# Optimization experiments

Hardware: AMD Instinct MI355X
Metric: run time of the kernel (lower is better)

The kernel has to match this reference:

```python
import jax, jax.numpy as jnp
import numpy as np

B, N, F_IN, F_HID, F_OUT = 64, 1024, 64, 128, 64

def setup_inputs() -> dict:
    key = jax.random.key(0)
    ks = jax.random.split(key, 6)
    x = jax.random.normal(ks[0], (B, N, F_IN), dtype=jnp.float32)
    adj = jax.random.uniform(ks[1], (B, N, N), dtype=jnp.float32)
    mask = jax.random.randint(ks[2], (B, N), 0, 2).astype(bool)
    W1 = jax.random.normal(ks[3], (F_IN, F_HID), dtype=jnp.float32) * (1.0 / np.sqrt(F_IN))
    b1 = jnp.zeros((F_HID,), dtype=jnp.float32)
    W2 = jax.random.normal(ks[4], (F_HID, F_OUT), dtype=jnp.float32) * (1.0 / np.sqrt(F_HID))
    b2 = jnp.zeros((F_OUT,), dtype=jnp.float32)
    eps = jnp.zeros((1,), dtype=jnp.float32)
    return {"x": x, "adj": adj, "mask": mask, "W1": W1, "b1": b1, "W2": W2, "b2": b2, "eps": eps}

def reference(x, adj, mask, W1, b1, W2, b2, eps):
    # neighbor aggregation: out[b,i,f] = sum_j adj[b,i,j] * x[b,j,f]
    agg = jnp.einsum('bij,bjf->bif', adj, x)
    # add_loop=True: (1 + eps) * x + aggregated neighbors
    h = (1.0 + eps[0]) * x + agg
    # 2-layer GIN MLP applied per node (only valid nodes contribute in the
    # torch version via gather/scatter; invalid positions are zeroed)
    h = jax.nn.relu(h @ W1 + b1) @ W2 + b2
    return jnp.where(mask[..., None], h, jnp.zeros((), dtype=h.dtype))
```

## Files before the change

### kernel.cpp

```cpp
#include <hip/hip_runtime.h>


#define N_    1024
#define FIN   64
#define FHID  128
#define FOUT  64
#define HS_LD 68
#define H1_LD 132
#define FROW  9

typedef __attribute__((ext_vector_type(16))) float f32x16;
typedef __attribute__((ext_vector_type(8)))  short s16x8;

__device__ inline short f2bf(float f) {
    union { float f; unsigned int u; } v; v.f = f;
    unsigned int r = v.u + 0x7fffu + ((v.u >> 16) & 1u);
    return (short)(r >> 16);
}

__global__ __launch_bounds__(256) void gin_fused(
    const float* __restrict__ x, const float* __restrict__ adj,
    const int* __restrict__ mask, const float* __restrict__ W1,
    const float* __restrict__ b1, const float* __restrict__ W2,
    const float* __restrict__ b2, const float* __restrict__ epsp,
    float* __restrict__ out)
{
    __shared__ s16x8 region1[2112];
    __shared__ float hs[64 * HS_LD];

    s16x8 (*asf)[FROW] = reinterpret_cast<s16x8 (*)[FROW]>(region1);
    s16x8 (*xtf)[FROW] = reinterpret_cast<s16x8 (*)[FROW]>(region1 + 576);
    float* h1s = reinterpret_cast<float*>(region1);

    const int t    = threadIdx.x;
    const int lane = t & 63;
    const int w    = t >> 6;
    const int b    = blockIdx.x >> 4;
    const int i0   = (blockIdx.x & 15) * 64;

    const float* xb   = x   + (size_t)b * N_ * FIN;
    const float* adjb = adj + (size_t)b * N_ * N_ + (size_t)i0 * N_;

    const int l31  = lane & 31;
    const int half = lane >> 5;
    const int mrow = (w & 1) * 32;
    const int ncol = (w >> 1) * 32;

    const int sr = t >> 2;
    const int sc = (t & 3) * 16;
    const int sg = (t & 3) * 2;

    f32x16 acc;
    #pragma unroll
    for (int r = 0; r < 16; ++r) acc[r] = 0.f;

    for (int jc = 0; jc < N_ / 64; ++jc) {
        const int j0 = jc * 64;

        {
            const float* ar = adjb + (size_t)sr * N_ + j0 + sc;
            const float4 p0 = *reinterpret_cast<const float4*>(ar);
            const float4 p1 = *reinterpret_cast<const float4*>(ar + 4);
            const float4 p2 = *reinterpret_cast<const float4*>(ar + 8);
            const float4 p3 = *reinterpret_cast<const float4*>(ar + 12);
            s16x8 f0, f1;
            f0[0] = f2bf(p0.x); f0[1] = f2bf(p0.y); f0[2] = f2bf(p0.z); f0[3] = f2bf(p0.w);
            f0[4] = f2bf(p1.x); f0[5] = f2bf(p1.y); f0[6] = f2bf(p1.z); f0[7] = f2bf(p1.w);
            f1[0] = f2bf(p2.x); f1[1] = f2bf(p2.y); f1[2] = f2bf(p2.z); f1[3] = f2bf(p2.w);
            f1[4] = f2bf(p3.x); f1[5] = f2bf(p3.y); f1[6] = f2bf(p3.z); f1[7] = f2bf(p3.w);
            asf[sr][sg]     = f0;
            asf[sr][sg + 1] = f1;
        }
        {
            s16x8 q0, q1;
            #pragma unroll
            for (int jj = 0; jj < 8; ++jj)
                q0[jj] = f2bf(xb[(size_t)(j0 + w * 16 + jj) * FIN + lane]);
            #pragma unroll
            for (int jj = 0; jj < 8; ++jj)
                q1[jj] = f2bf(xb[(size_t)(j0 + w * 16 + 8 + jj) * FIN + lane]);
            xtf[lane][2 * w]     = q0;
            xtf[lane][2 * w + 1] = q1;
        }
        __syncthreads();

        #pragma unroll
        for (int s = 0; s < 4; ++s) {
            const s16x8 a  = asf[mrow + l31][2 * s + half];
            const s16x8 bf = xtf[ncol + l31][2 * s + half];
            acc = __builtin_amdgcn_mfma_f32_32x32x16_bf16(a, bf, acc, 0, 0, 0);
        }
        __syncthreads();
    }

    {
        const float se = 1.0f + epsp[0];
        const int col = ncol + l31;
        #pragma unroll
        for (int reg = 0; reg < 16; ++reg) {
            const int row = mrow + (reg & 3) + 8 * (reg >> 2) + 4 * half;
            const float xv = xb[(size_t)(i0 + row) * FIN + col];
            hs[row * HS_LD + col] = acc[reg] + se * xv;
        }
    }
    __syncthreads();

    {
        const int k4 = (t & 31) * 4;
        const int rb = (t >> 5) * 8;
        float4 hacc[8];
        const float4 b1v = *reinterpret_cast<const float4*>(b1 + k4);
        #pragma unroll
        for (int r = 0; r < 8; ++r) hacc[r] = b1v;

        #pragma unroll 4
        for (int j = 0; j < FIN; ++j) {
            const float4 w1v = *reinterpret_cast<const float4*>(W1 + j * FHID + k4);
            #pragma unroll
            for (int r = 0; r < 8; ++r) {
                const float hv = hs[(rb + r) * HS_LD + j];
                hacc[r].x += hv * w1v.x; hacc[r].y += hv * w1v.y;
                hacc[r].z += hv * w1v.z; hacc[r].w += hv * w1v.w;
            }
        }
        #pragma unroll
        for (int r = 0; r < 8; ++r) {
            float4 v;
            v.x = fmaxf(hacc[r].x, 0.f); v.y = fmaxf(hacc[r].y, 0.f);
            v.z = fmaxf(hacc[r].z, 0.f); v.w = fmaxf(hacc[r].w, 0.f);
            *reinterpret_cast<float4*>(&h1s[(rb + r) * H1_LD + k4]) = v;
        }
    }
    __syncthreads();

    {
        const int fi = (t & 15) * 4;
        const int ri = (t >> 4) * 4;
        float4 oacc[4];
        const float4 b2v = *reinterpret_cast<const float4*>(b2 + fi);
        #pragma unroll
        for (int ii = 0; ii < 4; ++ii) oacc[ii] = b2v;

        #pragma unroll 4
        for (int j = 0; j < FHID; ++j) {
            const float4 w2v = *reinterpret_cast<const float4*>(W2 + j * FOUT + fi);
            #pragma unroll
            for (int ii = 0; ii < 4; ++ii) {
                const float hv = h1s[(ri + ii) * H1_LD + j];
                oacc[ii].x += hv * w2v.x; oacc[ii].y += hv * w2v.y;
                oacc[ii].z += hv * w2v.z; oacc[ii].w += hv * w2v.w;
            }
        }
        #pragma unroll
        for (int ii = 0; ii < 4; ++ii) {
            const int gi = i0 + ri + ii;
            const int m  = mask[b * N_ + gi];
            float4 o = oacc[ii];
            if (!m) o = make_float4(0.f, 0.f, 0.f, 0.f);
            *reinterpret_cast<float4*>(out + ((size_t)b * N_ + gi) * FOUT + fi) = o;
        }
    }
}

extern "C" void kernel_launch(void* const* d_in, const int* in_sizes, int n_in,
                              void* d_out, int out_size, void* d_ws, size_t ws_size,
                              hipStream_t stream) {
    const float* x    = (const float*)d_in[0];
    const float* adj  = (const float*)d_in[1];
    const int*   mask = (const int*)  d_in[2];
    const float* W1   = (const float*)d_in[3];
    const float* b1   = (const float*)d_in[4];
    const float* W2   = (const float*)d_in[5];
    const float* b2   = (const float*)d_in[6];
    const float* eps  = (const float*)d_in[7];
    float* out = (float*)d_out;

    dim3 grid(64 * 16);
    dim3 block(256);
    gin_fused<<<grid, block, 0, stream>>>(x, adj, mask, W1, b1, W2, b2, eps, out);
}
```

Measured before the change: 428.4 us.

## Pre-pack x and weights to bf16 fragments, stream adj directly, MFMA for MLP

Adds pre-pass kernels that convert x into transposed bf16 MFMA fragments and pack W1/W2 into bf16 fragments in workspace. The main kernel now loads adj straight from global memory into MFMA A-fragments, with no LDS staging and no per-chunk barriers. Both MLP layers move from scalar FP32 FMAs to bf16 MFMA, and launch bounds request higher occupancy. This removes redundant per-block x conversion and barrier stalls, but adds extra launches, workspace traffic and bf16 rounding in the MLP.

New measurement: 440.7 us. +2.9%, slower.

```diff
diff --git a/kernel.cpp b/kernel.cpp
--- a/kernel.cpp
+++ b/kernel.cpp
@@ -5,9 +5,7 @@
 #define FIN   64
 #define FHID  128
 #define FOUT  64
-#define HS_LD 68
-#define H1_LD 132
-#define FROW  9
+#define HROW  136
 
 typedef __attribute__((ext_vector_type(16))) float f32x16;
 typedef __attribute__((ext_vector_type(8)))  short s16x8;
@@ -18,19 +16,66 @@
     return (short)(r >> 16);
 }
 
-__global__ __launch_bounds__(256) void gin_fused(
+__global__ __launch_bounds__(256) void xt_pack(const float* __restrict__ x,
+                                               s16x8* __restrict__ xt)
+{
+    const int g  = blockIdx.x * 256 + threadIdx.x;
+    const int n  = g & 31;
+    const int ng = (g >> 5) & 1;
+    const int ks = (g >> 6) & 63;
+    const int b  = g >> 12;
+    const int f  = ng * 32 + n;
+
+    s16x8 u0, u1;
+    #pragma unroll
+    for (int k = 0; k < 8; ++k)
+        u0[k] = f2bf(x[(size_t)(b * N_ + ks * 16 + k) * FIN + f]);
+    #pragma unroll
+    for (int k = 0; k < 8; ++k)
+        u1[k] = f2bf(x[(size_t)(b * N_ + ks * 16 + 8 + k) * FIN + f]);
+    xt[2 * g]     = u0;
+    xt[2 * g + 1] = u1;
+}
+
+__global__ __launch_bounds__(256) void w_pack(const float* __restrict__ W1,
+                                              const float* __restrict__ W2,
+                                              s16x8* __restrict__ w1f,
+                                              s16x8* __restrict__ w2f)
+{
+    const int g = blockIdx.x * 256 + threadIdx.x;
+    const int u    = g & 63;
+    const int n    = u >> 1;
+    const int half = u & 1;
+    if (g < 1024) {
+        const int ng = (g >> 6) & 3;
+        const int ks = g >> 8;
+        s16x8 fr;
+        #pragma unroll
+        for (int e = 0; e < 8; ++e)
+            fr[e] = f2bf(W1[(16 * ks + 8 * half + e) * FHID + 32 * ng + n]);
+        w1f[g] = fr;
+    } else {
+        const int g2 = g - 1024;
+        const int ng = (g2 >> 6) & 1;
+        const int ks = g2 >> 7;
+        s16x8 fr;
+        #pragma unroll
+        for (int e = 0; e < 8; ++e)
+            fr[e] = f2bf(W2[(16 * ks + 8 * half + e) * FOUT + 32 * ng + n]);
+        w2f[g2] = fr;
+    }
+}
+
+__global__ __launch_bounds__(256, 4) void gin_main(
     const float* __restrict__ x, const float* __restrict__ adj,
-    const int* __restrict__ mask, const float* __restrict__ W1,
-    const float* __restrict__ b1, const float* __restrict__ W2,
+    const int* __restrict__ mask, const float* __restrict__ b1,
     const float* __restrict__ b2, const float* __restrict__ epsp,
-    float* __restrict__ out)
+    const s16x8* __restrict__ xt, const s16x8* __restrict__ w1f,
+    const s16x8* __restrict__ w2f, float* __restrict__ out)
 {
-    __shared__ s16x8 region1[2112];
-    __shared__ float hs[64 * HS_LD];
-
-    s16x8 (*asf)[FROW] = reinterpret_cast<s16x8 (*)[FROW]>(region1);
-    s16x8 (*xtf)[FROW] = reinterpret_cast<s16x8 (*)[FROW]>(region1 + 576);
-    float* h1s = reinterpret_cast<float*>(region1);
+    __shared__ unsigned short hf_hw[64 * HROW];
+    __shared__ unsigned short h1f_hw[64 * HROW];
+    __shared__ int mask_s[64];
 
     const int t    = threadIdx.x;
     const int lane = t & 63;
@@ -38,59 +83,31 @@
     const int b    = blockIdx.x >> 4;
     const int i0   = (blockIdx.x & 15) * 64;
 
-    const float* xb   = x   + (size_t)b * N_ * FIN;
-    const float* adjb = adj + (size_t)b * N_ * N_ + (size_t)i0 * N_;
-
     const int l31  = lane & 31;
     const int half = lane >> 5;
     const int mrow = (w & 1) * 32;
     const int ncol = (w >> 1) * 32;
-
-    const int sr = t >> 2;
-    const int sc = (t & 3) * 16;
-    const int sg = (t & 3) * 2;
+    const int bfl  = l31 * 2 + half;
+
+    if (t < 64) mask_s[t] = mask[b * N_ + i0 + t];
+
+    const float* ap = adj + (size_t)b * N_ * N_
+                          + (size_t)(i0 + mrow + l31) * N_ + 8 * half;
+    const s16x8* xb0 = xt + ((size_t)(b * 64) * 2 + (w >> 1)) * 64 + bfl;
 
     f32x16 acc;
     #pragma unroll
     for (int r = 0; r < 16; ++r) acc[r] = 0.f;
 
-    for (int jc = 0; jc < N_ / 64; ++jc) {
-        const int j0 = jc * 64;
-
-        {
-            const float* ar = adjb + (size_t)sr * N_ + j0 + sc;
-            const float4 p0 = *reinterpret_cast<const float4*>(ar);
-            const float4 p1 = *reinterpret_cast<const float4*>(ar + 4);
-            const float4 p2 = *reinterpret_cast<const float4*>(ar + 8);
-            const float4 p3 = *reinterpret_cast<const float4*>(ar + 12);
-            s16x8 f0, f1;
-            f0[0] = f2bf(p0.x); f0[1] = f2bf(p0.y); f0[2] = f2bf(p0.z); f0[3] = f2bf(p0.w);
-            f0[4] = f2bf(p1.x); f0[5] = f2bf(p1.y); f0[6] = f2bf(p1.z); f0[7] = f2bf(p1.w);
-            f1[0] = f2bf(p2.x); f1[1] = f2bf(p2.y); f1[2] = f2bf(p2.z); f1[3] = f2bf(p2.w);
-            f1[4] = f2bf(p3.x); f1[5] = f2bf(p3.y); f1[6] = f2bf(p3.z); f1[7] = f2bf(p3.w);
-            asf[sr][sg]     = f0;
-            asf[sr][sg + 1] = f1;
-        }
-        {
-            s16x8 q0, q1;
-            #pragma unroll
-            for (int jj = 0; jj < 8; ++jj)
-                q0[jj] = f2bf(xb[(size_t)(j0 + w * 16 + jj) * FIN + lane]);
-            #pragma unroll
-            for (int jj = 0; jj < 8; ++jj)
-                q1[jj] = f2bf(xb[(size_t)(j0 + w * 16 + 8 + jj) * FIN + lane]);
-            xtf[lane][2 * w]     = q0;
-            xtf[lane][2 * w + 1] = q1;
-        }
-        __syncthreads();
-
-        #pragma unroll
-        for (int s = 0; s < 4; ++s) {
-            const s16x8 a  = asf[mrow + l31][2 * s + half];
-            const s16x8 bf = xtf[ncol + l31][2 * s + half];
-            acc = __builtin_amdgcn_mfma_f32_32x32x16_bf16(a, bf, acc, 0, 0, 0);
-        }
-        __syncthreads();
+    #pragma unroll 8
+    for (int s = 0; s < 64; ++s) {
+        const float4 u = *reinterpret_cast<const float4*>(ap + 16 * s);
+        const float4 v = *reinterpret_cast<const float4*>(ap + 16 * s + 4);
+        const s16x8  bf = xb0[(size_t)s * 128];
+        s16x8 afr;
+        afr[0] = f2bf(u.x); afr[1] = f2bf(u.y); afr[2] = f2bf(u.z); afr[3] = f2bf(u.w);
+        afr[4] = f2bf(v.x); afr[5] = f2bf(v.y); afr[6] = f2bf(v.z); afr[7] = f2bf(v.w);
+        acc = __builtin_amdgcn_mfma_f32_32x32x16_bf16(afr, bf, acc, 0, 0, 0);
     }
 
     {
@@ -99,65 +116,63 @@
         #pragma unroll
         for (int reg = 0; reg < 16; ++reg) {
             const int row = mrow + (reg & 3) + 8 * (reg >> 2) + 4 * half;
-            const float xv = xb[(size_t)(i0 + row) * FIN + col];
-            hs[row * HS_LD + col] = acc[reg] + se * xv;
+            const float xv = x[(size_t)(b * N_ + i0 + row) * FIN + col];
+            hf_hw[row * HROW + col] = (unsigned short)f2bf(acc[reg] + se * xv);
         }
     }
     __syncthreads();
 
     {
-        const int k4 = (t & 31) * 4;
-        const int rb = (t >> 5) * 8;
-        float4 hacc[8];
-        const float4 b1v = *reinterpret_cast<const float4*>(b1 + k4);
-        #pragma unroll
-        for (int r = 0; r < 8; ++r) hacc[r] = b1v;
-
-        #pragma unroll 4
-        for (int j = 0; j < FIN; ++j) {
-            const float4 w1v = *reinterpret_cast<const float4*>(W1 + j * FHID + k4);
+        f32x16 acc2[2];
+        #pragma unroll
+        for (int g = 0; g < 2; ++g) {
+            const float b1v = b1[32 * (2 * (w >> 1) + g) + l31];
             #pragma unroll
-            for (int r = 0; r < 8; ++r) {
-                const float hv = hs[(rb + r) * HS_LD + j];
-                hacc[r].x += hv * w1v.x; hacc[r].y += hv * w1v.y;
-                hacc[r].z += hv * w1v.z; hacc[r].w += hv * w1v.w;
+            for (int r = 0; r < 16; ++r) acc2[g][r] = b1v;
+        }
+        #pragma unroll
+        for (int s = 0; s < 4; ++s) {
+            const s16x8 a = *reinterpret_cast<const s16x8*>(
+                &hf_hw[(mrow + l31) * HROW + 16 * s + 8 * half]);
+            #pragma unroll
+            for (int g = 0; g < 2; ++g) {
+                const int ngB = 2 * (w >> 1) + g;
+                const s16x8 bw = w1f[(s * 4 + ngB) * 64 + bfl];
+                acc2[g] = __builtin_amdgcn_mfma_f32_32x32x16_bf16(a, bw, acc2[g], 0, 0, 0);
             }
         }
         #pragma unroll
-        for (int r = 0; r < 8; ++r) {
-            float4 v;
-            v.x = fmaxf(hacc[r].x, 0.f); v.y = fmaxf(hacc[r].y, 0.f);
-            v.z = fmaxf(hacc[r].z, 0.f); v.w = fmaxf(hacc[r].w, 0.f);
-            *reinterpret_cast<float4*>(&h1s[(rb + r) * H1_LD + k4]) = v;
+        for (int g = 0; g < 2; ++g) {
+            const int col = 32 * (2 * (w >> 1) + g) + l31;
+            #pragma unroll
+            for (int reg = 0; reg < 16; ++reg) {
+                const int row = mrow + (reg & 3) + 8 * (reg >> 2) + 4 * half;
+                h1f_hw[row * HROW + col] = (unsigned short)f2bf(fmaxf(acc2[g][reg], 0.f));
+            }
         }
     }
     __syncthreads();
 
     {
-        const int fi = (t & 15) * 4;
-        const int ri = (t >> 4) * 4;
-        float4 oacc[4];
-        const float4 b2v = *reinterpret_cast<const float4*>(b2 + fi);
-        #pragma unroll
-        for (int ii = 0; ii < 4; ++ii) oacc[ii] = b2v;
-
-        #pragma unroll 4
-        for (int j = 0; j < FHID; ++j) {
-            const float4 w2v = *reinterpret_cast<const float4*>(W2 + j * FOUT + fi);
-            #pragma unroll
-            for (int ii = 0; ii < 4; ++ii) {
-                const float hv = h1s[(ri + ii) * H1_LD + j];
-                oacc[ii].x += hv * w2v.x; oacc[ii].y += hv * w2v.y;
-                oacc[ii].z += hv * w2v.z; oacc[ii].w += hv * w2v.w;
-            }
-        }
-        #pragma unroll
-        for (int ii = 0; ii < 4; ++ii) {
-            const int gi = i0 + ri + ii;
-            const int m  = mask[b * N_ + gi];
-            float4 o = oacc[ii];
-            if (!m) o = make_float4(0.f, 0.f, 0.f, 0.f);
-            *reinterpret_cast<float4*>(out + ((size_t)b * N_ + gi) * FOUT + fi) = o;
+        f32x16 acc3;
+        const float b2v = b2[ncol + l31];
+        #pragma unroll
+        for (int r = 0; r < 16; ++r) acc3[r] = b2v;
+
+        #pragma unroll
+        for (int s = 0; s < 8; ++s) {
+            const s16x8 a = *reinterpret_cast<const s16x8*>(
+                &h1f_hw[(mrow + l31) * HROW + 16 * s + 8 * half]);
+            const s16x8 bw = w2f[(s * 2 + (w >> 1)) * 64 + bfl];
+            acc3 = __builtin_amdgcn_mfma_f32_32x32x16_bf16(a, bw, acc3, 0, 0, 0);
+        }
+
+        const int col = ncol + l31;
+        #pragma unroll
+        for (int reg = 0; reg < 16; ++reg) {
+            const int row = mrow + (reg & 3) + 8 * (reg >> 2) + 4 * half;
+            const float o = mask_s[row] ? acc3[reg] : 0.f;
+            out[(size_t)(b * N_ + i0 + row) * FOUT + col] = o;
         }
     }
 }
@@ -175,7 +190,12 @@
     const float* eps  = (const float*)d_in[7];
     float* out = (float*)d_out;
 
-    dim3 grid(64 * 16);
-    dim3 block(256);
-    gin_fused<<<grid, block, 0, stream>>>(x, adj, mask, W1, b1, W2, b2, eps, out);
-}
+    s16x8* xt  = (s16x8*)d_ws;
+    s16x8* w1f = xt + 524288;
+    s16x8* w2f = w1f + 1024;
+
+    xt_pack<<<dim3(1024), dim3(256), 0, stream>>>(x, xt);
+    w_pack<<<dim3(8), dim3(256), 0, stream>>>(W1, W2, w1f, w2f);
+    gin_main<<<dim3(64 * 16), dim3(256), 0, stream>>>(x, adj, mask, b1, b2, eps,
+                                                      xt, w1f, w2f, out);
+}
```
